# Optimization experiments

Hardware: AMD Instinct MI355X
Metric: run time of the kernel (lower is better)

## Reference

```python
import jax, jax.numpy as jnp
import numpy as np

DIM = 512
EXP = 2
INNER = EXP * DIM            # 1024
QKV_BLOCK = 64
NH = INNER // QKV_BLOCK      # 16 heads
DH = QKV_BLOCK               # 64 head dim
B, S = 2, 2048
KSZ = 4                      # causal conv kernel size
EPS = 5e-5                   # backend eps
NORM_EPS = 1e-6
CAP = 15.0                   # gate soft cap


def setup_inputs() -> dict:
    key = jax.random.key(0)
    ks = jax.random.split(key, 10)
    sc = lambda d: (2.0 / (5.0 * d)) ** 0.5  # small_init std
    b_if = jnp.concatenate([jnp.zeros(NH), jnp.linspace(3.0, 6.0, NH)]).astype(jnp.float32)
    return {
        "x": jax.random.normal(ks[0], (B, S, DIM), jnp.float32),
        "W_up": (jax.random.normal(ks[1], (2 * INNER, DIM), jnp.float32) * sc(DIM)),
        "W_q": (jax.random.normal(ks[2], (NH, DH, DH), jnp.float32) * sc(DH)),
        "W_k": (jax.random.normal(ks[3], (NH, DH, DH), jnp.float32) * sc(DH)),
        "W_v": (jax.random.normal(ks[4], (NH, DH, DH), jnp.float32) * sc(DH)),
        "conv_w": (jax.random.normal(ks[5], (INNER, KSZ), jnp.float32) * (1.0 / KSZ ** 0.5)),
        "conv_b": jnp.zeros((INNER,), jnp.float32),
        "W_if": (jax.random.normal(ks[6], (2 * NH, 3 * INNER), jnp.float32) * 0.02),
        "b_if": b_if,
        "norm_w": jnp.zeros((INNER,), jnp.float32),  # residual weight: gain = 1 + w
        "skip": jnp.ones((INNER,), jnp.float32),
        "W_down": (jax.random.normal(ks[7], (DIM, INNER), jnp.float32) * (2.0 / 15.0 / INNER ** 0.5)),
    }


def _headwise(x, W):
    # x: (B,S,INNER) -> per-head block-diagonal projection with W: (NH,DH,DH)
    xh = x.reshape(*x.shape[:-1], NH, DH)
    yh = jnp.einsum('bsnd,nod->bsno', xh, W)
    return yh.reshape(*x.shape[:-1], INNER)


def _causal_conv1d(x, w, b):
    # depthwise causal conv along S; x: (B,S,C), w: (C,K), b: (C,)
    xp = jnp.pad(x, ((0, 0), (KSZ - 1, 0), (0, 0)))
    y = b
    for j in range(KSZ):  # fixed tiny kernel loop
        y = y + xp[:, j:j + S, :] * w[:, j]
    return y


def _mlstm_parallel(q, k, v, i, f):
    # q,k,v: (B,NH,S,DH); i,f: (B,NH,S). Stabilized parallel mLSTM (native chunkwise math).
    logf = jax.nn.log_sigmoid(f)
    Fc = jnp.cumsum(logf, axis=-1)                              # (B,NH,S)
    logD = Fc[:, :, :, None] - Fc[:, :, None, :] + i[:, :, None, :]
    mask = jnp.tril(jnp.ones((S, S), bool))
    logD = jnp.where(mask, logD, -jnp.inf)
    m = jnp.max(logD, axis=-1)                                  # (B,NH,S), finite (diag = i[t])
    D = jnp.exp(logD - m[..., None])
    Smat = jnp.einsum('bnsd,bntd->bnst', q, k) * (DH ** -0.5)
    C = Smat * D
    n = jnp.maximum(jnp.abs(C.sum(axis=-1)), jnp.exp(-m))       # normalizer
    return jnp.einsum('bnst,bntd->bnsd', C, v) / (n + EPS)[..., None]


def reference(x, W_up, W_q, W_k, W_v, conv_w, conv_b, W_if, b_if, norm_w, skip, W_down):
    # up-projection and gate split
    x_inner = jnp.einsum('bsd,ed->bse', x, W_up)                # (B,S,2*INNER)
    x_mlstm, z = x_inner[..., :INNER], x_inner[..., INNER:]

    # causal depthwise conv + SiLU
    x_conv_act = jax.nn.silu(_causal_conv1d(x_mlstm, conv_w, conv_b))

    # headwise q,k,v
    q = _headwise(x_conv_act, W_q)
    k = _headwise(x_conv_act, W_k)
    v = _headwise(x_mlstm, W_v)

    # gate preactivations with soft cap
    if_pre = jnp.einsum('bse,ge->bsg', jnp.concatenate([q, k, v], axis=-1), W_if) + b_if
    if_pre = CAP * jnp.tanh(if_pre / CAP)
    i_pre, f_pre = if_pre[..., :NH], if_pre[..., NH:]           # (B,S,NH)
    i_g = i_pre.transpose(0, 2, 1)                              # (B,NH,S)
    f_g = f_pre.transpose(0, 2, 1)

    qh = q.reshape(B, S, NH, DH).transpose(0, 2, 1, 3)
    kh = k.reshape(B, S, NH, DH).transpose(0, 2, 1, 3)
    vh = v.reshape(B, S, NH, DH).transpose(0, 2, 1, 3)

    h = _mlstm_parallel(qh, kh, vh, i_g, f_g)                   # (B,NH,S,DH)

    # multi-head RMSNorm with residual gain (1 + w)
    rrms = jax.lax.rsqrt(jnp.mean(h * h, axis=-1, keepdims=True) + NORM_EPS)
    gain = (1.0 + norm_w).reshape(1, NH, 1, DH)
    h_norm = (h * rrms * gain).transpose(0, 2, 1, 3).reshape(B, S, INNER)

    # learnable skip, output gate, down-projection
    h_tilde = h_norm + skip * x_conv_act
    h_out = h_tilde * jax.nn.silu(z)
    return jnp.einsum('bse,de->bsd', h_out, W_down)
```

## Files before the change

kernel.cpp:

```cpp
#include <hip/hip_runtime.h>
#include <math.h>

constexpr int DIM_   = 512;
constexpr int INNER_ = 1024;
constexpr int NHEAD  = 16;
constexpr int BATCH  = 2;
constexpr int SEQ_   = 2048;
constexpr int TOK    = BATCH * SEQ_;
constexpr float EPS_ = 5e-5f;
constexpr float NEPS = 1e-6f;
constexpr float CAPV = 15.0f;

typedef __bf16 bf16_t;
typedef __attribute__((ext_vector_type(8)))  __bf16 bf16x8;
typedef __attribute__((ext_vector_type(4)))  __bf16 bf16x4;
typedef __attribute__((ext_vector_type(16))) float  f32x16;
typedef __attribute__((ext_vector_type(4)))  unsigned int u32x4;

template<int BM, int BN, int WM, int WN, int MODE>
__global__ __launch_bounds__(256) void gemm_split(const float* __restrict__ A,
    const float* __restrict__ B, float* __restrict__ C,
    int K, int lda, int ldb, int ldc)
{
    constexpr bool HAS_AL = (MODE >= 2), HAS_BL = (MODE >= 3);
    constexpr int TM = WM / 32, TN = WN / 32, NWC = BN / WN;
    __shared__ __align__(16) bf16_t sAh[BM * 32];
    __shared__ __align__(16) bf16_t sBh[BN * 32];
    __shared__ __align__(16) bf16_t sAl[HAS_AL ? BM * 32 : 8];
    __shared__ __align__(16) bf16_t sBl[HAS_BL ? BN * 32 : 8];
    const int bm = blockIdx.y * BM, bn = blockIdx.x * BN;
    const int tid = threadIdx.x, w = tid >> 6, l = tid & 63;
    const int l31 = l & 31, lh = l >> 5;
    const int wr = w / NWC, wc = w % NWC;
    f32x16 acc[TM][TN];
#pragma unroll
    for (int i = 0; i < TM; ++i)
#pragma unroll
        for (int j = 0; j < TN; ++j)
#pragma unroll
            for (int r = 0; r < 16; ++r) acc[i][j][r] = 0.f;

    for (int k0 = 0; k0 < K; k0 += 32) {
#pragma unroll
        for (int it = 0; it < BM * 4 / 256; ++it) {
            int gi = tid + it * 256; int row = gi >> 2, g = gi & 3;
            const float* src = A + (size_t)(bm + row) * lda + k0 + g * 8;
            float4 u0 = *(const float4*)src, u1 = *(const float4*)(src + 4);
            float va[8] = {u0.x, u0.y, u0.z, u0.w, u1.x, u1.y, u1.z, u1.w};
            bf16x8 h, lo2;
#pragma unroll
            for (int e = 0; e < 8; ++e) {
                bf16_t hv = (bf16_t)va[e]; h[e] = hv;
                if constexpr (HAS_AL) lo2[e] = (bf16_t)(va[e] - (float)hv);
            }
            int off = row * 32 + ((g ^ (row & 3)) << 3);
            *(bf16x8*)&sAh[off] = h;
            if constexpr (HAS_AL) *(bf16x8*)&sAl[off] = lo2;
        }
#pragma unroll
        for (int it = 0; it < BN * 4 / 256; ++it) {
            int gi = tid + it * 256; int row = gi >> 2, g = gi & 3;
            const float* src = B + (size_t)(bn + row) * ldb + k0 + g * 8;
            float4 u0 = *(const float4*)src, u1 = *(const float4*)(src + 4);
            float va[8] = {u0.x, u0.y, u0.z, u0.w, u1.x, u1.y, u1.z, u1.w};
            bf16x8 h, lo2;
#pragma unroll
            for (int e = 0; e < 8; ++e) {
                bf16_t hv = (bf16_t)va[e]; h[e] = hv;
                if constexpr (HAS_BL) lo2[e] = (bf16_t)(va[e] - (float)hv);
            }
            int off = row * 32 + ((g ^ (row & 3)) << 3);
            *(bf16x8*)&sBh[off] = h;
            if constexpr (HAS_BL) *(bf16x8*)&sBl[off] = lo2;
        }
        __syncthreads();
#pragma unroll
        for (int ks = 0; ks < 2; ++ks) {
            const int gk = 2 * ks + lh;
            bf16x8 af[TM], alf[TM], bfv[TN], blf[TN];
#pragma unroll
            for (int i = 0; i < TM; ++i) {
                int row = wr * WM + i * 32 + l31;
                int off = row * 32 + ((gk ^ (row & 3)) << 3);
                af[i] = *(const bf16x8*)&sAh[off];
                if constexpr (HAS_AL) alf[i] = *(const bf16x8*)&sAl[off];
            }
#pragma unroll
            for (int j = 0; j < TN; ++j) {
                int row = wc * WN + j * 32 + l31;
                int off = row * 32 + ((gk ^ (row & 3)) << 3);
                bfv[j] = *(const bf16x8*)&sBh[off];
                if constexpr (HAS_BL) blf[j] = *(const bf16x8*)&sBl[off];
            }
#pragma unroll
            for (int i = 0; i < TM; ++i)
#pragma unroll
                for (int j = 0; j < TN; ++j) {
                    acc[i][j] = __builtin_amdgcn_mfma_f32_32x32x16_bf16(af[i], bfv[j], acc[i][j], 0, 0, 0);
                    if constexpr (HAS_AL)
                        acc[i][j] = __builtin_amdgcn_mfma_f32_32x32x16_bf16(alf[i], bfv[j], acc[i][j], 0, 0, 0);
                    if constexpr (HAS_BL)
                        acc[i][j] = __builtin_amdgcn_mfma_f32_32x32x16_bf16(af[i], blf[j], acc[i][j], 0, 0, 0);
                }
        }
        __syncthreads();
    }
#pragma unroll
    for (int i = 0; i < TM; ++i)
#pragma unroll
        for (int j = 0; j < TN; ++j)
#pragma unroll
            for (int r = 0; r < 16; ++r) {
                int row = bm + wr * WM + i * 32 + (r & 3) + 8 * (r >> 2) + 4 * lh;
                int col = bn + wc * WN + j * 32 + l31;
                C[(size_t)row * ldc + col] = acc[i][j][r];
            }
}

__global__ __launch_bounds__(256) void conv_silu_k(const float* __restrict__ xin,
    const float* __restrict__ cw, const float* __restrict__ cb, float* __restrict__ xca)
{
    const int c = blockIdx.x * 256 + threadIdx.x;
    const int t = blockIdx.y;
    const int s = t & (SEQ_ - 1);
    const float w0 = cw[c*4+0], w1 = cw[c*4+1], w2 = cw[c*4+2], w3 = cw[c*4+3];
    const float* base = xin + (size_t)t * 2048 + c;
    float acc = cb[c];
    if (s >= 3) acc += base[-3*2048] * w0;
    if (s >= 2) acc += base[-2*2048] * w1;
    if (s >= 1) acc += base[-1*2048] * w2;
    acc += base[0] * w3;
    float sg = 1.f / (1.f + __expf(-acc));
    xca[(size_t)t * INNER_ + c] = acc * sg;
}

__global__ __launch_bounds__(256) void wif_cvt(const float* __restrict__ W_if,
    bf16_t* __restrict__ wif16)
{
    int i4 = blockIdx.x * 256 + threadIdx.x;
    float4 v = *(const float4*)(W_if + (size_t)i4 * 4);
    bf16x4 o; o[0]=(bf16_t)v.x; o[1]=(bf16_t)v.y; o[2]=(bf16_t)v.z; o[3]=(bf16_t)v.w;
    *(bf16x4*)(wif16 + (size_t)i4 * 4) = o;
}

__global__ __launch_bounds__(256) void qkv_mfma(const float* __restrict__ xca,
    const float* __restrict__ xin, const float* __restrict__ Wq,
    const float* __restrict__ Wk, const float* __restrict__ Wv,
    bf16_t* __restrict__ qb16, bf16_t* __restrict__ kb16,
    bf16_t* __restrict__ vb16, bf16_t* __restrict__ vbt16)
{
    __shared__ __align__(16) bf16_t Xs[128 * 64];
    __shared__ __align__(16) bf16_t Ws[64 * 64];
    const int mt = blockIdx.x, n = blockIdx.y, which = blockIdx.z;
    const int t0 = mt * 128, b = t0 >> 11, s0 = t0 & (SEQ_ - 1);
    const float* X = (which == 2) ? xin : xca;
    const size_t xpitch = (which == 2) ? 2048 : 1024;
    const float* W = ((which == 0) ? Wq : (which == 1) ? Wk : Wv) + n * 4096;
    const int tid = threadIdx.x, w = tid >> 6, l = tid & 63, l31 = l & 31, lh = l >> 5;
    const size_t gbn = (size_t)(b * NHEAD + n) * SEQ_;

#pragma unroll
    for (int it = 0; it < 4; ++it) {
        int gi = tid + it * 256; int row = gi >> 3, g = gi & 7;
        const float* src = X + (size_t)(t0 + row) * xpitch + n * 64 + g * 8;
        float4 u0 = *(const float4*)src, u1 = *(const float4*)(src + 4);
        float va[8] = {u0.x, u0.y, u0.z, u0.w, u1.x, u1.y, u1.z, u1.w};
        bf16x8 h;
#pragma unroll
        for (int e = 0; e < 8; ++e) h[e] = (bf16_t)va[e];
        *(bf16x8*)&Xs[row * 64 + ((g ^ (row & 7)) << 3)] = h;
    }
#pragma unroll
    for (int it = 0; it < 2; ++it) {
        int gi = tid + it * 256; int row = gi >> 3, g = gi & 7;
        const float* src = W + row * 64 + g * 8;
        float4 u0 = *(const float4*)src, u1 = *(const float4*)(src + 4);
        float va[8] = {u0.x, u0.y, u0.z, u0.w, u1.x, u1.y, u1.z, u1.w};
        bf16x8 h;
#pragma unroll
        for (int e = 0; e < 8; ++e) h[e] = (bf16_t)va[e];
        *(bf16x8*)&Ws[row * 64 + ((g ^ (row & 7)) << 3)] = h;
    }
    __syncthreads();

    if (which < 2) {
        const int wr = w >> 1, wc = w & 1;
        f32x16 acc[2];
#pragma unroll
        for (int i = 0; i < 2; ++i)
#pragma unroll
            for (int r = 0; r < 16; ++r) acc[i][r] = 0.f;
#pragma unroll
        for (int ks = 0; ks < 4; ++ks) {
            const int gk = 2 * ks + lh;
            const int wrow = wc * 32 + l31;
            bf16x8 bfrag = *(const bf16x8*)&Ws[wrow * 64 + ((gk ^ (wrow & 7)) << 3)];
#pragma unroll
            for (int i = 0; i < 2; ++i) {
                int row = wr * 64 + i * 32 + l31;
                bf16x8 afrag = *(const bf16x8*)&Xs[row * 64 + ((gk ^ (row & 7)) << 3)];
                acc[i] = __builtin_amdgcn_mfma_f32_32x32x16_bf16(afrag, bfrag, acc[i], 0, 0, 0);
            }
        }
        bf16_t* dst = which ? kb16 : qb16;
#pragma unroll
        for (int i = 0; i < 2; ++i)
#pragma unroll
            for (int r = 0; r < 16; ++r) {
                int srow = wr * 64 + i * 32 + (r & 3) + 8 * (r >> 2) + 4 * lh;
                dst[(gbn + s0 + srow) * 64 + wc * 32 + l31] = (bf16_t)acc[i][r];
            }
    } else {
        const int dh = w >> 1, th = w & 1;
        f32x16 acc[2];
#pragma unroll
        for (int j = 0; j < 2; ++j)
#pragma unroll
            for (int r = 0; r < 16; ++r) acc[j][r] = 0.f;
#pragma unroll
        for (int ks = 0; ks < 4; ++ks) {
            const int gk = 2 * ks + lh;
            const int wrow = dh * 32 + l31;
            bf16x8 afrag = *(const bf16x8*)&Ws[wrow * 64 + ((gk ^ (wrow & 7)) << 3)];
#pragma unroll
            for (int j = 0; j < 2; ++j) {
                int xrow = th * 64 + j * 32 + l31;
                bf16x8 bfrag = *(const bf16x8*)&Xs[xrow * 64 + ((gk ^ (xrow & 7)) << 3)];
                acc[j] = __builtin_amdgcn_mfma_f32_32x32x16_bf16(afrag, bfrag, acc[j], 0, 0, 0);
            }
        }
        const size_t vtb = (size_t)(b * NHEAD + n) * 64;
#pragma unroll
        for (int j = 0; j < 2; ++j)
#pragma unroll
            for (int r = 0; r < 16; ++r) {
                int drow = dh * 32 + (r & 3) + 8 * (r >> 2) + 4 * lh;
                int tcol = th * 64 + j * 32 + l31;
                vbt16[(vtb + drow) * SEQ_ + s0 + tcol] = (bf16_t)acc[j][r];
            }
        __syncthreads();
#pragma unroll
        for (int j = 0; j < 2; ++j)
#pragma unroll
            for (int r = 0; r < 16; ++r) {
                int tokrow = th * 64 + j * 32 + l31;
                int d = dh * 32 + (r & 3) + 8 * (r >> 2) + 4 * lh;
                Xs[tokrow * 64 + ((((d >> 3) ^ (tokrow & 7))) << 3) + (d & 7)] = (bf16_t)acc[j][r];
            }
        __syncthreads();
#pragma unroll
        for (int it = 0; it < 4; ++it) {
            int gi = tid + it * 256; int row = gi >> 3, g = gi & 7;
            bf16x8 v = *(const bf16x8*)&Xs[row * 64 + ((g ^ (row & 7)) << 3)];
            *(bf16x8*)&vb16[(gbn + s0 + row) * 64 + g * 8] = v;
        }
    }
}

__global__ __launch_bounds__(256) void if_mfma(const bf16_t* __restrict__ qb16,
    const bf16_t* __restrict__ kb16, const bf16_t* __restrict__ vb16,
    const bf16_t* __restrict__ wif16, float* __restrict__ ifp)
{
    __shared__ float red[4][32][33];
    const int t0g = blockIdx.x * 32;
    const int b = t0g >> 11, s0 = t0g & (SEQ_ - 1);
    const int tid = threadIdx.x, w = tid >> 6, l = tid & 63, l31 = l & 31, lh = l >> 5;
    const size_t base0 = (size_t)b * NHEAD * SEQ_ * 64 + (size_t)(s0 + l31) * 64;
    const bf16_t* wbase = wif16 + (size_t)l31 * 3072 + 8 * lh;
    f32x16 acc;
#pragma unroll
    for (int r = 0; r < 16; ++r) acc[r] = 0.f;
#pragma unroll 4
    for (int it = 0; it < 48; ++it) {
        const int kg = w * 768 + it * 16;
        const int which = kg >> 10, rem = kg & 1023;
        const int head = rem >> 6, dd = (rem & 63) + 8 * lh;
        const bf16_t* src = (which == 0) ? qb16 : (which == 1) ? kb16 : vb16;
        bf16x8 af = *(const bf16x8*)(src + base0 + (size_t)head * SEQ_ * 64 + dd);
        bf16x8 bf = *(const bf16x8*)(wbase + kg);
        acc = __builtin_amdgcn_mfma_f32_32x32x16_bf16(af, bf, acc, 0, 0, 0);
    }
#pragma unroll
    for (int r = 0; r < 16; ++r) {
        int row = (r & 3) + 8 * (r >> 2) + 4 * lh;
        red[w][row][l31] = acc[r];
    }
    __syncthreads();
#pragma unroll
    for (int it = 0; it < 4; ++it) {
        int idx = tid + it * 256;
        int row = idx >> 5, col = idx & 31;
        float s = red[0][row][col] + red[1][row][col] + red[2][row][col] + red[3][row][col];
        ifp[(size_t)(t0g + row) * 32 + col] = s;
    }
}

__global__ __launch_bounds__(256) void gate_scan(const float* __restrict__ ifp,
    const float* __restrict__ b_if, float* __restrict__ colfac,
    float* __restrict__ cmaxv, float* __restrict__ emv)
{
    __shared__ float tots[256];
    __shared__ float cmE[32];
    const int bn = blockIdx.x;
    const int b = bn >> 4, n = bn & 15;
    const int tid = threadIdx.x;
    const float bi = b_if[n], bf = b_if[16 + n];
    const int s0 = tid * 8;
    float iv[8], lf[8];
#pragma unroll
    for (int j = 0; j < 8; ++j) {
        size_t row = ((size_t)b * SEQ_ + s0 + j) * 32;
        float ip = ifp[row + n] + bi;        ip = CAPV * tanhf(ip * (1.f / CAPV));
        float fp = ifp[row + 16 + n] + bf;   fp = CAPV * tanhf(fp * (1.f / CAPV));
        float ls = fminf(fp, 0.f) - log1pf(expf(-fabsf(fp)));
        iv[j] = ip; lf[j] = ls;
    }
#pragma unroll
    for (int j = 1; j < 8; ++j) lf[j] += lf[j-1];
    tots[tid] = lf[7];
    __syncthreads();
    for (int off = 1; off < 256; off <<= 1) {
        float o = (tid >= off) ? tots[tid - off] : 0.f;
        __syncthreads();
        tots[tid] += o;
        __syncthreads();
    }
    const float exs = (tid > 0) ? tots[tid - 1] : 0.f;
    float Fc[8], a[8], am[8];
#pragma unroll
    for (int j = 0; j < 8; ++j) { Fc[j] = exs + lf[j]; a[j] = iv[j] - Fc[j]; }
    am[0] = a[0];
#pragma unroll
    for (int j = 1; j < 8; ++j) am[j] = fmaxf(am[j-1], a[j]);
    __syncthreads();
    tots[tid] = am[7];
    __syncthreads();
    for (int off = 1; off < 256; off <<= 1) {
        float o = (tid >= off) ? tots[tid - off] : -INFINITY;
        __syncthreads();
        tots[tid] = fmaxf(tots[tid], o);
        __syncthreads();
    }
    const float exm = (tid > 0) ? tots[tid - 1] : -INFINITY;
    if ((tid & 7) == 7) cmE[tid >> 3] = fmaxf(exm, am[7]);
    __syncthreads();
    const float ce = cmE[tid >> 3];
    const size_t base = (size_t)bn * SEQ_ + s0;
#pragma unroll
    for (int j = 0; j < 8; ++j) {
        float cm = fmaxf(exm, am[j]);
        colfac[base + j] = __expf(a[j] - ce);
        cmaxv[base + j]  = cm;
        emv[base + j]    = expf(-(Fc[j] + cm));
    }
}

__global__ __launch_bounds__(256) void kscale(bf16_t* __restrict__ kb16,
    const float* __restrict__ colfac)
{
    const int i = blockIdx.x * 256 + threadIdx.x;
    const int row = i >> 3, c = (i & 7) << 3;
    const float cf = 0.125f * colfac[row];
    bf16x8 v = *(const bf16x8*)(kb16 + (size_t)row * 64 + c);
#pragma unroll
    for (int e = 0; e < 8; ++e) v[e] = (bf16_t)((float)v[e] * cf);
    *(bf16x8*)(kb16 + (size_t)row * 64 + c) = v;
}

__device__ inline unsigned pack2(float a, float b) {
    union { bf16_t h; unsigned short u; } ua, ub;
    ua.h = (bf16_t)a; ub.h = (bf16_t)b;
    return (unsigned)ua.u | ((unsigned)ub.u << 16);
}

__global__ __launch_bounds__(256, 3) void mlstm_k3(
    const bf16_t* __restrict__ qb16, const bf16_t* __restrict__ khat,
    const bf16_t* __restrict__ vbt16,
    const float* __restrict__ cmaxv, const float* __restrict__ emv,
    const float* __restrict__ xca, const float* __restrict__ xin,
    const float* __restrict__ norm_w, const float* __restrict__ skipv,
    float* __restrict__ houtp)
{
    __shared__ __align__(16) bf16_t ks[2][64*64];
    __shared__ __align__(16) bf16_t vts[2][64*64];
    __shared__ float cmB_sh[32];
    __shared__ float inv_lds[64];
    __shared__ float red_lds[2][2][2][16];

    const int bid = blockIdx.x;
    const int r8 = bid & 7, rem = bid >> 3;
    const int jj = rem & 31, qq = rem >> 5;
    const int bnh = r8 + 8 * qq;
    const int b = bnh >> 4, n = bnh & 15;
    const int st = 31 - jj;

    const int tid = threadIdx.x, w = tid >> 6, l = tid & 63;
    const int l31 = l & 31, lh = l >> 5;
    const int sh = w >> 1, dh = w & 1;
    const size_t gb = (size_t)(b * NHEAD + n) * SEQ_;
    const int s_lane = 32 * sh + l31;
    const int d_lane = 32 * dh + l31;

    const float cmq = cmaxv[gb + (size_t)st * 64 + s_lane];
    const float emq = emv[gb + (size_t)st * 64 + s_lane];
    const int col = n * 64 + d_lane;
    const float gn = 1.f + norm_w[col];
    const float sk = skipv[col];
    if (tid < 32) cmB_sh[tid] = cmaxv[gb + (size_t)tid * 64 + 63];

    bf16x8 qf[4];
    {
        const bf16_t* qp = qb16 + (gb + (size_t)st * 64 + s_lane) * 64 + 8 * lh;
#pragma unroll
        for (int kc = 0; kc < 4; ++kc) qf[kc] = *(const bf16x8*)(qp + 16 * kc);
    }
    f32x16 hac;
#pragma unroll
    for (int i = 0; i < 16; ++i) hac[i] = 0.f;
    float csum = 0.f;

    const bf16_t* kbase = khat + gb * 64;
    const bf16_t* vbase = vbt16 + (size_t)(b * NHEAD + n) * 64 * SEQ_;

#define STAGE(buf, ttv) { \
    const bf16_t* kgp = kbase + (size_t)(ttv) * 64 * 64; \
    const bf16_t* vgp = vbase + (size_t)(ttv) * 64; \
    _Pragma("unroll") \
    for (int it_ = 0; it_ < 2; ++it_) { \
        int id_ = tid + it_ * 256; \
        int r_ = id_ >> 3, c_ = (id_ & 7) << 3; \
        int sw_ = c_ ^ ((r_ & 7) << 3); \
        *(bf16x8*)&ks[buf][r_ * 64 + sw_] = *(const bf16x8*)(kgp + r_ * 64 + c_); \
        *(bf16x8*)&vts[buf][r_ * 64 + sw_] = *(const bf16x8*)(vgp + (size_t)r_ * SEQ_ + c_); \
    } }

    STAGE(0, 0)
    int cur = 0;
    for (int tt = 0; tt <= st; ++tt) {
        __syncthreads();
        if (tt < st) STAGE(cur ^ 1, tt + 1)
        const float rf = __expf(cmB_sh[tt] - cmq);
        const bool diag = (tt == st);
#pragma unroll
        for (int tq = 0; tq < 2; ++tq) {
            if (diag && sh == 0 && tq == 1) continue;
            f32x16 p;
#pragma unroll
            for (int i = 0; i < 16; ++i) p[i] = 0.f;
            const int krow = 32 * tq + l31;
            const int swk = (krow & 7) << 3;
#pragma unroll
            for (int kc = 0; kc < 4; ++kc) {
                bf16x8 kf = *(const bf16x8*)&ks[cur][krow * 64 + ((8 * lh + 16 * kc) ^ swk)];
                p = __builtin_amdgcn_mfma_f32_32x32x16_bf16(kf, qf[kc], p, 0, 0, 0);
            }
#pragma unroll
            for (int reg = 0; reg < 16; ++reg) {
                const int t_loc = (reg & 3) + 8 * (reg >> 2) + 4 * lh + 32 * tq;
                float pw = p[reg] * rf;
                if (diag && t_loc > s_lane) pw = 0.f;
                csum += pw;
                p[reg] = pw;
            }
            unsigned W0 = pack2(p[0],  p[1]),  W1 = pack2(p[2],  p[3]);
            unsigned W2 = pack2(p[4],  p[5]),  W3 = pack2(p[6],  p[7]);
            unsigned W4 = pack2(p[8],  p[9]),  W5 = pack2(p[10], p[11]);
            unsigned W6 = pack2(p[12], p[13]), W7 = pack2(p[14], p[15]);
            unsigned r1 = __shfl_xor(lh ? W0 : W2, 32, 64);
            unsigned r2 = __shfl_xor(lh ? W1 : W3, 32, 64);
            unsigned r3 = __shfl_xor(lh ? W4 : W6, 32, 64);
            unsigned r4 = __shfl_xor(lh ? W5 : W7, 32, 64);
            u32x4 pa0 = lh ? (u32x4){r1, r2, W2, W3} : (u32x4){W0, W1, r1, r2};
            u32x4 pa1 = lh ? (u32x4){r3, r4, W6, W7} : (u32x4){W4, W5, r3, r4};
            const int swv = (d_lane & 7) << 3;
#pragma unroll
            for (int kcl = 0; kcl < 2; ++kcl) {
                const int kcg = 2 * tq + kcl;
                bf16x8 vf = *(const bf16x8*)&vts[cur][d_lane * 64 + ((8 * lh + 16 * kcg) ^ swv)];
                bf16x8 paf = __builtin_bit_cast(bf16x8, kcl ? pa1 : pa0);
                hac = __builtin_amdgcn_mfma_f32_32x32x16_bf16(paf, vf, hac, 0, 0, 0);
            }
        }
        cur ^= 1;
    }
#undef STAGE

    csum += __shfl_xor(csum, 32, 64);
    const float ivv = 1.f / (fmaxf(fabsf(csum), emq) + EPS_);
    if (dh == 0 && lh == 0) inv_lds[s_lane] = ivv;
    __syncthreads();
    float sq[16];
#pragma unroll
    for (int reg = 0; reg < 16; ++reg) {
        const int s_loc = (reg & 3) + 8 * (reg >> 2) + 4 * lh;
        float h = hac[reg] * inv_lds[32 * sh + s_loc];
        hac[reg] = h;
        float s2 = h * h;
        s2 += __shfl_xor(s2, 1);  s2 += __shfl_xor(s2, 2);
        s2 += __shfl_xor(s2, 4);  s2 += __shfl_xor(s2, 8);
        s2 += __shfl_xor(s2, 16);
        sq[reg] = s2;
    }
    if (l31 == 0) {
#pragma unroll
        for (int reg = 0; reg < 16; ++reg) red_lds[sh][dh][lh][reg] = sq[reg];
    }
    __syncthreads();
#pragma unroll
    for (int reg = 0; reg < 16; ++reg) {
        const int s_loc = (reg & 3) + 8 * (reg >> 2) + 4 * lh;
        const float ssq = red_lds[sh][0][lh][reg] + red_lds[sh][1][lh][reg];
        const float rr = rsqrtf(ssq * (1.f / 64.f) + NEPS);
        const size_t tok = (size_t)b * SEQ_ + (size_t)st * 64 + 32 * sh + s_loc;
        float ht = hac[reg] * rr * gn + sk * xca[tok * INNER_ + col];
        float zz = xin[tok * 2048 + 1024 + col];
        float sil = zz / (1.f + __expf(-zz));
        houtp[tok * 2048 + col] = ht * sil;
    }
}

extern "C" void kernel_launch(void* const* d_in, const int* in_sizes, int n_in,
                              void* d_out, int out_size, void* d_ws, size_t ws_size,
                              hipStream_t stream)
{
    const float* x      = (const float*)d_in[0];
    const float* W_up   = (const float*)d_in[1];
    const float* W_q    = (const float*)d_in[2];
    const float* W_k    = (const float*)d_in[3];
    const float* W_v    = (const float*)d_in[4];
    const float* conv_w = (const float*)d_in[5];
    const float* conv_b = (const float*)d_in[6];
    const float* W_if   = (const float*)d_in[7];
    const float* b_if   = (const float*)d_in[8];
    const float* norm_w = (const float*)d_in[9];
    const float* skip   = (const float*)d_in[10];
    const float* W_down = (const float*)d_in[11];
    float* out = (float*)d_out;

    float* xin    = (float*)d_ws;
    float* xca    = xin  + (size_t)TOK * 2048;
    float* ifp    = xca  + (size_t)TOK * INNER_;
    float* colfac = ifp  + (size_t)TOK * 32;
    float* cmaxv  = colfac + (size_t)BATCH * NHEAD * SEQ_;
    float* emv    = cmaxv  + (size_t)BATCH * NHEAD * SEQ_;
    bf16_t* qb16  = (bf16_t*)(emv + (size_t)BATCH * NHEAD * SEQ_);
    bf16_t* kb16  = qb16 + (size_t)TOK * INNER_;
    bf16_t* vb16  = kb16 + (size_t)TOK * INNER_;
    bf16_t* vbt16 = vb16 + (size_t)TOK * INNER_;
    bf16_t* wif16 = vbt16+ (size_t)TOK * INNER_;

    gemm_split<128,128,64,64,3><<<dim3(2048/128, TOK/128), 256, 0, stream>>>(
        x, W_up, xin, DIM_, DIM_, DIM_, 2048);
    conv_silu_k<<<dim3(INNER_/256, TOK), 256, 0, stream>>>(xin, conv_w, conv_b, xca);
    wif_cvt<<<dim3(96), 256, 0, stream>>>(W_if, wif16);
    qkv_mfma<<<dim3(TOK/128, NHEAD, 3), 256, 0, stream>>>(xca, xin, W_q, W_k, W_v,
        qb16, kb16, vb16, vbt16);
    if_mfma<<<dim3(TOK/32), 256, 0, stream>>>(qb16, kb16, vb16, wif16, ifp);
    gate_scan<<<dim3(BATCH*NHEAD), 256, 0, stream>>>(ifp, b_if, colfac, cmaxv, emv);
    kscale<<<dim3(TOK*INNER_/8/256), 256, 0, stream>>>(kb16, colfac);
    mlstm_k3<<<dim3(1024), 256, 0, stream>>>(qb16, kb16, vbt16,
        cmaxv, emv, xca, xin, norm_w, skip, xin );
    gemm_split<128,64,32,64,2><<<dim3(DIM_/64, TOK/128), 256, 0, stream>>>(
        xin, W_down, out, INNER_, 2048, INNER_, DIM_);
}
```

Measured before the change: 290.5 us.

## Fold headwise QKV weights into gate projection and compute row sums via MFMA

Precomposes W_if with the headwise q/k/v weights into a 32x2048 bf16 matrix, so gate preactivations come straight from the conv activations and the x_mlstm input. This drops the token-major v buffer and its LDS transpose from the qkv kernel. The mLSTM kernel now gets the normalizer row sums from an extra MFMA against a ones vector instead of scalar accumulation and a shuffle, and its occupancy hint rises to 4. Composing the weights in fp32 and rounding once to bf16 changes the rounding of the gate inputs. The extra MFMA per step adds matrix-core work in the hot loop.

```diff
diff --git a/kernel.cpp b/kernel.cpp
--- a/kernel.cpp
+++ b/kernel.cpp
@@ -134,20 +134,144 @@
     xca[(size_t)t * INNER_ + c] = acc * sg;
 }
 
-__global__ __launch_bounds__(256) void wif_cvt(const float* __restrict__ W_if,
-    bf16_t* __restrict__ wif16)
-{
-    int i4 = blockIdx.x * 256 + threadIdx.x;
-    float4 v = *(const float4*)(W_if + (size_t)i4 * 4);
-    bf16x4 o; o[0]=(bf16_t)v.x; o[1]=(bf16_t)v.y; o[2]=(bf16_t)v.z; o[3]=(bf16_t)v.w;
-    *(bf16x4*)(wif16 + (size_t)i4 * 4) = o;
+__global__ __launch_bounds__(256) void mcompose(const float* __restrict__ Wq,
+    const float* __restrict__ Wk, const float* __restrict__ Wv,
+    const float* __restrict__ Wif, bf16_t* __restrict__ m16)
+{
+    const int n = blockIdx.x;
+    const int tid = threadIdx.x;
+    const int g = tid >> 3, d0 = (tid & 7) << 3;
+    float aq[8] = {}, av[8] = {};
+    const float* wifq = Wif + (size_t)g * 3072 + n * 64;
+    const float* wifk = wifq + 1024;
+    const float* wifv = wifq + 2048;
+    const float* wqb = Wq + n * 4096;
+    const float* wkb = Wk + n * 4096;
+    const float* wvb = Wv + n * 4096;
+    for (int o = 0; o < 64; ++o) {
+        float cq = wifq[o], ck = wifk[o], cv = wifv[o];
+        const float* q4 = wqb + o * 64 + d0;
+        const float* k4 = wkb + o * 64 + d0;
+        const float* v4 = wvb + o * 64 + d0;
+#pragma unroll
+        for (int e = 0; e < 8; ++e) {
+            aq[e] += cq * q4[e] + ck * k4[e];
+            av[e] += cv * v4[e];
+        }
+    }
+    bf16x8 oq, ov;
+#pragma unroll
+    for (int e = 0; e < 8; ++e) { oq[e] = (bf16_t)aq[e]; ov[e] = (bf16_t)av[e]; }
+    *(bf16x8*)(m16 + (size_t)g * 2048 + n * 64 + d0) = oq;
+    *(bf16x8*)(m16 + (size_t)g * 2048 + 1024 + n * 64 + d0) = ov;
+}
+
+__global__ __launch_bounds__(512) void if_mfma2(const float* __restrict__ xca,
+    const float* __restrict__ xin, const bf16_t* __restrict__ m16,
+    float* __restrict__ ifp)
+{
+    __shared__ float red[8][32][33];
+    const int t0g = blockIdx.x * 32;
+    const int tid = threadIdx.x, w = tid >> 6, l = tid & 63, l31 = l & 31, lh = l >> 5;
+    const int tok = t0g + l31;
+    const bf16_t* mbase = m16 + (size_t)l31 * 2048 + 8 * lh;
+    f32x16 acc;
+#pragma unroll
+    for (int r = 0; r < 16; ++r) acc[r] = 0.f;
+    const int kw = w * 256;
+#pragma unroll 4
+    for (int it = 0; it < 16; ++it) {
+        const int ksub = kw + it * 16 + 8 * lh;
+        const float* ap = (ksub < 1024) ? (xca + (size_t)tok * 1024 + ksub)
+                                        : (xin + (size_t)tok * 2048 + (ksub - 1024));
+        float4 u0 = *(const float4*)ap, u1 = *(const float4*)(ap + 4);
+        bf16x8 af;
+        af[0] = (bf16_t)u0.x; af[1] = (bf16_t)u0.y; af[2] = (bf16_t)u0.z; af[3] = (bf16_t)u0.w;
+        af[4] = (bf16_t)u1.x; af[5] = (bf16_t)u1.y; af[6] = (bf16_t)u1.z; af[7] = (bf16_t)u1.w;
+        bf16x8 bf = *(const bf16x8*)(mbase + kw + it * 16);
+        acc = __builtin_amdgcn_mfma_f32_32x32x16_bf16(af, bf, acc, 0, 0, 0);
+    }
+#pragma unroll
+    for (int r = 0; r < 16; ++r) {
+        int row = (r & 3) + 8 * (r >> 2) + 4 * lh;
+        red[w][row][l31] = acc[r];
+    }
+    __syncthreads();
+#pragma unroll
+    for (int it = 0; it < 2; ++it) {
+        int idx = tid + it * 512;
+        int row = idx >> 5, colg = idx & 31;
+        float s = 0.f;
+#pragma unroll
+        for (int ww = 0; ww < 8; ++ww) s += red[ww][row][colg];
+        ifp[(size_t)(t0g + row) * 32 + colg] = s;
+    }
+}
+
+__global__ __launch_bounds__(256) void gate_scan(const float* __restrict__ ifp,
+    const float* __restrict__ b_if, float* __restrict__ colfac,
+    float* __restrict__ cmaxv, float* __restrict__ emv)
+{
+    __shared__ float tots[256];
+    __shared__ float cmE[32];
+    const int bn = blockIdx.x;
+    const int b = bn >> 4, n = bn & 15;
+    const int tid = threadIdx.x;
+    const float bi = b_if[n], bf = b_if[16 + n];
+    const int s0 = tid * 8;
+    float iv[8], lf[8];
+#pragma unroll
+    for (int j = 0; j < 8; ++j) {
+        size_t row = ((size_t)b * SEQ_ + s0 + j) * 32;
+        float ip = ifp[row + n] + bi;        ip = CAPV * tanhf(ip * (1.f / CAPV));
+        float fp = ifp[row + 16 + n] + bf;   fp = CAPV * tanhf(fp * (1.f / CAPV));
+        float ls = fminf(fp, 0.f) - log1pf(expf(-fabsf(fp)));
+        iv[j] = ip; lf[j] = ls;
+    }
+#pragma unroll
+    for (int j = 1; j < 8; ++j) lf[j] += lf[j-1];
+    tots[tid] = lf[7];
+    __syncthreads();
+    for (int off = 1; off < 256; off <<= 1) {
+        float o = (tid >= off) ? tots[tid - off] : 0.f;
+        __syncthreads();
+        tots[tid] += o;
+        __syncthreads();
+    }
+    const float exs = (tid > 0) ? tots[tid - 1] : 0.f;
+    float Fc[8], a[8], am[8];
+#pragma unroll
+    for (int j = 0; j < 8; ++j) { Fc[j] = exs + lf[j]; a[j] = iv[j] - Fc[j]; }
+    am[0] = a[0];
+#pragma unroll
+    for (int j = 1; j < 8; ++j) am[j] = fmaxf(am[j-1], a[j]);
+    __syncthreads();
+    tots[tid] = am[7];
+    __syncthreads();
+    for (int off = 1; off < 256; off <<= 1) {
+        float o = (tid >= off) ? tots[tid - off] : -INFINITY;
+        __syncthreads();
+        tots[tid] = fmaxf(tots[tid], o);
+        __syncthreads();
+    }
+    const float exm = (tid > 0) ? tots[tid - 1] : -INFINITY;
+    if ((tid & 7) == 7) cmE[tid >> 3] = fmaxf(exm, am[7]);
+    __syncthreads();
+    const float ce = cmE[tid >> 3];
+    const size_t base = (size_t)bn * SEQ_ + s0;
+#pragma unroll
+    for (int j = 0; j < 8; ++j) {
+        float cm = fmaxf(exm, am[j]);
+        colfac[base + j] = __expf(a[j] - ce);
+        cmaxv[base + j]  = cm;
+        emv[base + j]    = expf(-(Fc[j] + cm));
+    }
 }
 
 __global__ __launch_bounds__(256) void qkv_mfma(const float* __restrict__ xca,
     const float* __restrict__ xin, const float* __restrict__ Wq,
     const float* __restrict__ Wk, const float* __restrict__ Wv,
-    bf16_t* __restrict__ qb16, bf16_t* __restrict__ kb16,
-    bf16_t* __restrict__ vb16, bf16_t* __restrict__ vbt16)
+    bf16_t* __restrict__ qb16, bf16_t* __restrict__ kb16, bf16_t* __restrict__ vbt16)
 {
     __shared__ __align__(16) bf16_t Xs[128 * 64];
     __shared__ __align__(16) bf16_t Ws[64 * 64];
@@ -238,120 +362,6 @@
                 int tcol = th * 64 + j * 32 + l31;
                 vbt16[(vtb + drow) * SEQ_ + s0 + tcol] = (bf16_t)acc[j][r];
             }
-        __syncthreads();
-#pragma unroll
-        for (int j = 0; j < 2; ++j)
-#pragma unroll
-            for (int r = 0; r < 16; ++r) {
-                int tokrow = th * 64 + j * 32 + l31;
-                int d = dh * 32 + (r & 3) + 8 * (r >> 2) + 4 * lh;
-                Xs[tokrow * 64 + ((((d >> 3) ^ (tokrow & 7))) << 3) + (d & 7)] = (bf16_t)acc[j][r];
-            }
-        __syncthreads();
-#pragma unroll
-        for (int it = 0; it < 4; ++it) {
-            int gi = tid + it * 256; int row = gi >> 3, g = gi & 7;
-            bf16x8 v = *(const bf16x8*)&Xs[row * 64 + ((g ^ (row & 7)) << 3)];
-            *(bf16x8*)&vb16[(gbn + s0 + row) * 64 + g * 8] = v;
-        }
-    }
-}
-
-__global__ __launch_bounds__(256) void if_mfma(const bf16_t* __restrict__ qb16,
-    const bf16_t* __restrict__ kb16, const bf16_t* __restrict__ vb16,
-    const bf16_t* __restrict__ wif16, float* __restrict__ ifp)
-{
-    __shared__ float red[4][32][33];
-    const int t0g = blockIdx.x * 32;
-    const int b = t0g >> 11, s0 = t0g & (SEQ_ - 1);
-    const int tid = threadIdx.x, w = tid >> 6, l = tid & 63, l31 = l & 31, lh = l >> 5;
-    const size_t base0 = (size_t)b * NHEAD * SEQ_ * 64 + (size_t)(s0 + l31) * 64;
-    const bf16_t* wbase = wif16 + (size_t)l31 * 3072 + 8 * lh;
-    f32x16 acc;
-#pragma unroll
-    for (int r = 0; r < 16; ++r) acc[r] = 0.f;
-#pragma unroll 4
-    for (int it = 0; it < 48; ++it) {
-        const int kg = w * 768 + it * 16;
-        const int which = kg >> 10, rem = kg & 1023;
-        const int head = rem >> 6, dd = (rem & 63) + 8 * lh;
-        const bf16_t* src = (which == 0) ? qb16 : (which == 1) ? kb16 : vb16;
-        bf16x8 af = *(const bf16x8*)(src + base0 + (size_t)head * SEQ_ * 64 + dd);
-        bf16x8 bf = *(const bf16x8*)(wbase + kg);
-        acc = __builtin_amdgcn_mfma_f32_32x32x16_bf16(af, bf, acc, 0, 0, 0);
-    }
-#pragma unroll
-    for (int r = 0; r < 16; ++r) {
-        int row = (r & 3) + 8 * (r >> 2) + 4 * lh;
-        red[w][row][l31] = acc[r];
-    }
-    __syncthreads();
-#pragma unroll
-    for (int it = 0; it < 4; ++it) {
-        int idx = tid + it * 256;
-        int row = idx >> 5, col = idx & 31;
-        float s = red[0][row][col] + red[1][row][col] + red[2][row][col] + red[3][row][col];
-        ifp[(size_t)(t0g + row) * 32 + col] = s;
-    }
-}
-
-__global__ __launch_bounds__(256) void gate_scan(const float* __restrict__ ifp,
-    const float* __restrict__ b_if, float* __restrict__ colfac,
-    float* __restrict__ cmaxv, float* __restrict__ emv)
-{
-    __shared__ float tots[256];
-    __shared__ float cmE[32];
-    const int bn = blockIdx.x;
-    const int b = bn >> 4, n = bn & 15;
-    const int tid = threadIdx.x;
-    const float bi = b_if[n], bf = b_if[16 + n];
-    const int s0 = tid * 8;
-    float iv[8], lf[8];
-#pragma unroll
-    for (int j = 0; j < 8; ++j) {
-        size_t row = ((size_t)b * SEQ_ + s0 + j) * 32;
-        float ip = ifp[row + n] + bi;        ip = CAPV * tanhf(ip * (1.f / CAPV));
-        float fp = ifp[row + 16 + n] + bf;   fp = CAPV * tanhf(fp * (1.f / CAPV));
-        float ls = fminf(fp, 0.f) - log1pf(expf(-fabsf(fp)));
-        iv[j] = ip; lf[j] = ls;
-    }
-#pragma unroll
-    for (int j = 1; j < 8; ++j) lf[j] += lf[j-1];
-    tots[tid] = lf[7];
-    __syncthreads();
-    for (int off = 1; off < 256; off <<= 1) {
-        float o = (tid >= off) ? tots[tid - off] : 0.f;
-        __syncthreads();
-        tots[tid] += o;
-        __syncthreads();
-    }
-    const float exs = (tid > 0) ? tots[tid - 1] : 0.f;
-    float Fc[8], a[8], am[8];
-#pragma unroll
-    for (int j = 0; j < 8; ++j) { Fc[j] = exs + lf[j]; a[j] = iv[j] - Fc[j]; }
-    am[0] = a[0];
-#pragma unroll
-    for (int j = 1; j < 8; ++j) am[j] = fmaxf(am[j-1], a[j]);
-    __syncthreads();
-    tots[tid] = am[7];
-    __syncthreads();
-    for (int off = 1; off < 256; off <<= 1) {
-        float o = (tid >= off) ? tots[tid - off] : -INFINITY;
-        __syncthreads();
-        tots[tid] = fmaxf(tots[tid], o);
-        __syncthreads();
-    }
-    const float exm = (tid > 0) ? tots[tid - 1] : -INFINITY;
-    if ((tid & 7) == 7) cmE[tid >> 3] = fmaxf(exm, am[7]);
-    __syncthreads();
-    const float ce = cmE[tid >> 3];
-    const size_t base = (size_t)bn * SEQ_ + s0;
-#pragma unroll
-    for (int j = 0; j < 8; ++j) {
-        float cm = fmaxf(exm, am[j]);
-        colfac[base + j] = __expf(a[j] - ce);
-        cmaxv[base + j]  = cm;
-        emv[base + j]    = expf(-(Fc[j] + cm));
     }
 }
 
@@ -373,7 +383,7 @@
     return (unsigned)ua.u | ((unsigned)ub.u << 16);
 }
 
-__global__ __launch_bounds__(256, 3) void mlstm_k3(
+__global__ __launch_bounds__(256, 4) void mlstm_k3b(
     const bf16_t* __restrict__ qb16, const bf16_t* __restrict__ khat,
     const bf16_t* __restrict__ vbt16,
     const float* __restrict__ cmaxv, const float* __restrict__ emv,
@@ -384,7 +394,7 @@
     __shared__ __align__(16) bf16_t ks[2][64*64];
     __shared__ __align__(16) bf16_t vts[2][64*64];
     __shared__ float cmB_sh[32];
-    __shared__ float inv_lds[64];
+    __shared__ float em_sh[64];
     __shared__ float red_lds[2][2][2][16];
 
     const int bid = blockIdx.x;
@@ -402,11 +412,11 @@
     const int d_lane = 32 * dh + l31;
 
     const float cmq = cmaxv[gb + (size_t)st * 64 + s_lane];
-    const float emq = emv[gb + (size_t)st * 64 + s_lane];
     const int col = n * 64 + d_lane;
     const float gn = 1.f + norm_w[col];
     const float sk = skipv[col];
     if (tid < 32) cmB_sh[tid] = cmaxv[gb + (size_t)tid * 64 + 63];
+    if (tid < 64) em_sh[tid] = emv[gb + (size_t)st * 64 + tid];
 
     bf16x8 qf[4];
     {
@@ -414,10 +424,13 @@
 #pragma unroll
         for (int kc = 0; kc < 4; ++kc) qf[kc] = *(const bf16x8*)(qp + 16 * kc);
     }
-    f32x16 hac;
-#pragma unroll
-    for (int i = 0; i < 16; ++i) hac[i] = 0.f;
-    float csum = 0.f;
+    bf16x8 onesf;
+#pragma unroll
+    for (int e = 0; e < 8; ++e) onesf[e] = (bf16_t)1.0f;
+
+    f32x16 hac, cs;
+#pragma unroll
+    for (int i = 0; i < 16; ++i) { hac[i] = 0.f; cs[i] = 0.f; }
 
     const bf16_t* kbase = khat + gb * 64;
     const bf16_t* vbase = vbt16 + (size_t)(b * NHEAD + n) * 64 * SEQ_;
@@ -459,7 +472,6 @@
                 const int t_loc = (reg & 3) + 8 * (reg >> 2) + 4 * lh + 32 * tq;
                 float pw = p[reg] * rf;
                 if (diag && t_loc > s_lane) pw = 0.f;
-                csum += pw;
                 p[reg] = pw;
             }
             unsigned W0 = pack2(p[0],  p[1]),  W1 = pack2(p[2],  p[3]);
@@ -479,21 +491,19 @@
                 bf16x8 vf = *(const bf16x8*)&vts[cur][d_lane * 64 + ((8 * lh + 16 * kcg) ^ swv)];
                 bf16x8 paf = __builtin_bit_cast(bf16x8, kcl ? pa1 : pa0);
                 hac = __builtin_amdgcn_mfma_f32_32x32x16_bf16(paf, vf, hac, 0, 0, 0);
+                cs  = __builtin_amdgcn_mfma_f32_32x32x16_bf16(paf, onesf, cs, 0, 0, 0);
             }
         }
         cur ^= 1;
     }
 #undef STAGE
 
-    csum += __shfl_xor(csum, 32, 64);
-    const float ivv = 1.f / (fmaxf(fabsf(csum), emq) + EPS_);
-    if (dh == 0 && lh == 0) inv_lds[s_lane] = ivv;
-    __syncthreads();
     float sq[16];
 #pragma unroll
     for (int reg = 0; reg < 16; ++reg) {
         const int s_loc = (reg & 3) + 8 * (reg >> 2) + 4 * lh;
-        float h = hac[reg] * inv_lds[32 * sh + s_loc];
+        const float den = fmaxf(fabsf(cs[reg]), em_sh[32 * sh + s_loc]) + EPS_;
+        float h = hac[reg] / den;
         hac[reg] = h;
         float s2 = h * h;
         s2 += __shfl_xor(s2, 1);  s2 += __shfl_xor(s2, 2);
@@ -545,20 +555,19 @@
     float* emv    = cmaxv  + (size_t)BATCH * NHEAD * SEQ_;
     bf16_t* qb16  = (bf16_t*)(emv + (size_t)BATCH * NHEAD * SEQ_);
     bf16_t* kb16  = qb16 + (size_t)TOK * INNER_;
-    bf16_t* vb16  = kb16 + (size_t)TOK * INNER_;
-    bf16_t* vbt16 = vb16 + (size_t)TOK * INNER_;
-    bf16_t* wif16 = vbt16+ (size_t)TOK * INNER_;
+    bf16_t* vbt16 = kb16 + (size_t)TOK * INNER_;
+    bf16_t* m16   = vbt16 + (size_t)TOK * INNER_;
 
     gemm_split<128,128,64,64,3><<<dim3(2048/128, TOK/128), 256, 0, stream>>>(
         x, W_up, xin, DIM_, DIM_, DIM_, 2048);
     conv_silu_k<<<dim3(INNER_/256, TOK), 256, 0, stream>>>(xin, conv_w, conv_b, xca);
-    wif_cvt<<<dim3(96), 256, 0, stream>>>(W_if, wif16);
+    mcompose<<<dim3(NHEAD), 256, 0, stream>>>(W_q, W_k, W_v, W_if, m16);
+    if_mfma2<<<dim3(TOK/32), 512, 0, stream>>>(xca, xin, m16, ifp);
+    gate_scan<<<dim3(BATCH*NHEAD), 256, 0, stream>>>(ifp, b_if, colfac, cmaxv, emv);
     qkv_mfma<<<dim3(TOK/128, NHEAD, 3), 256, 0, stream>>>(xca, xin, W_q, W_k, W_v,
-        qb16, kb16, vb16, vbt16);
-    if_mfma<<<dim3(TOK/32), 256, 0, stream>>>(qb16, kb16, vb16, wif16, ifp);
-    gate_scan<<<dim3(BATCH*NHEAD), 256, 0, stream>>>(ifp, b_if, colfac, cmaxv, emv);
+        qb16, kb16, vbt16);
     kscale<<<dim3(TOK*INNER_/8/256), 256, 0, stream>>>(kb16, colfac);
-    mlstm_k3<<<dim3(1024), 256, 0, stream>>>(qb16, kb16, vbt16,
+    mlstm_k3b<<<dim3(1024), 256, 0, stream>>>(qb16, kb16, vbt16,
         cmaxv, emv, xca, xin, norm_w, skip, xin );
     gemm_split<128,64,32,64,2><<<dim3(DIM_/64, TOK/128), 256, 0, stream>>>(
         xin, W_down, out, INNER_, 2048, INNER_, DIM_);
```

Measured after the change: 322.8 us. +11.1%, slower.
